# Kernel optimization log

Hardware: AMD Instinct MI355X
Metric: run time of the kernel (lower is better)

## Reference

```python
import jax, jax.numpy as jnp
import numpy as np
import math

B, S, H = 2, 2048, 2048
NQ, NKV, HD = 16, 4, 128
THETA = 10000.0


def rotate_half(x):
    x1, x2 = jnp.split(x, 2, axis=-1)
    return jnp.concatenate([-x2, x1], axis=-1)


def rope_cos_sin(position_ids, dim, base, dtype):
    # inv_freq: (dim/2,)
    inv_freq = 1.0 / (base ** (jnp.arange(0, dim, 2, dtype=jnp.float32) / dim))
    freqs = position_ids.astype(jnp.float32)[..., None] * inv_freq  # (B, S, dim/2)
    emb = jnp.concatenate([freqs, freqs], axis=-1)  # (B, S, dim)
    return jnp.cos(emb).astype(dtype), jnp.sin(emb).astype(dtype)


def setup_inputs() -> dict:
    key = jax.random.key(0)
    ks = jax.random.split(key, 5)
    hidden_states = jax.random.normal(ks[0], (B, S, H), dtype=jnp.float32)
    position_ids = jnp.broadcast_to(jnp.arange(S, dtype=jnp.int32)[None, :], (B, S))
    sc = 0.02
    wq = jax.random.normal(ks[1], (NQ * HD, H), dtype=jnp.float32) * sc
    wk = jax.random.normal(ks[2], (NKV * HD, H), dtype=jnp.float32) * sc
    wv = jax.random.normal(ks[3], (NKV * HD, H), dtype=jnp.float32) * sc
    wo = jax.random.normal(ks[4], (H, NQ * HD), dtype=jnp.float32) * sc
    return {"hidden_states": hidden_states, "position_ids": position_ids,
            "wq": wq, "wk": wk, "wv": wv, "wo": wo}


def reference(hidden_states, position_ids, wq, wk, wv, wo):
    b, s, _ = hidden_states.shape
    n_rep = NQ // NKV
    # QKV projections (no bias)
    q = (hidden_states @ wq.T).reshape(b, s, NQ, HD).transpose(0, 2, 1, 3)   # (b, nq, s, hd)
    k = (hidden_states @ wk.T).reshape(b, s, NKV, HD).transpose(0, 2, 1, 3)  # (b, nkv, s, hd)
    v = (hidden_states @ wv.T).reshape(b, s, NKV, HD).transpose(0, 2, 1, 3)
    # RoPE (full rotary, partial_rotary_factor == 1.0)
    cos, sin = rope_cos_sin(position_ids, HD, THETA, q.dtype)  # (b, s, hd)
    cos = cos[:, None, :, :]
    sin = sin[:, None, :, :]
    q = q * cos + rotate_half(q) * sin
    k = k * cos + rotate_half(k) * sin
    # repeat_kv for GQA: (b, nkv, s, hd) -> (b, nq, s, hd)
    k = jnp.repeat(k, n_rep, axis=1)
    v = jnp.repeat(v, n_rep, axis=1)
    # scores (b, nq, s, s)
    scores = jnp.einsum('bhqd,bhkd->bhqk', q, k) / math.sqrt(HD)
    causal = jnp.triu(jnp.full((s, s), -jnp.inf, dtype=scores.dtype), k=1)
    scores = scores + causal
    probs = jax.nn.softmax(scores.astype(jnp.float32), axis=-1).astype(q.dtype)
    out = jnp.einsum('bhqk,bhkd->bhqd', probs, v)  # (b, nq, s, hd)
    out = out.transpose(0, 2, 1, 3).reshape(b, s, NQ * HD)
    return out @ wo.T
```

## Files before the change

### kernel.cpp

```cpp
#include <hip/hip_runtime.h>
#include <hip/hip_bf16.h>
#include <cstdint>

typedef unsigned short u16;
typedef __attribute__((ext_vector_type(4))) float f32x4;
typedef __attribute__((ext_vector_type(8))) short s16x8;
typedef __attribute__((ext_vector_type(4))) unsigned int u32x4;
typedef __attribute__((ext_vector_type(2))) unsigned int u32x2;
typedef __attribute__((ext_vector_type(4))) unsigned short u16x4;

#define MFMA16(a, b, c) __builtin_amdgcn_mfma_f32_16x16x32_bf16(a, b, c, 0, 0, 0)
#define GLOAD16(g, l) __builtin_amdgcn_global_load_lds((const __attribute__((address_space(1))) void*)(g), (__attribute__((address_space(3))) void*)(l), 16, 0, 0)

__device__ __forceinline__ u16 f2bf(float f) {
    union { float f; uint32_t u; } v{f};
    uint32_t r = v.u + 0x7FFF + ((v.u >> 16) & 1);
    return (u16)(r >> 16);
}

__global__ void cast_f32_bf16(const float* __restrict__ in, u16* __restrict__ out, int n4) {
    int i = blockIdx.x * 256 + threadIdx.x;
    if (i >= n4) return;
    float4 f = ((const float4*)in)[i];
    u16x4 o = { f2bf(f.x), f2bf(f.y), f2bf(f.z), f2bf(f.w) };
    ((u16x4*)out)[i] = o;
}

__global__ void rope_table_k(const int* __restrict__ pos, float* __restrict__ ct, float* __restrict__ st) {
    int i = blockIdx.x * 256 + threadIdx.x;
    int j = i & 63;
    int bs = i >> 6;
    float p = (float)pos[bs];
    float invf = powf(10000.0f, -(float)j * (1.0f / 64.0f));
    float ang = p * invf;
    ct[i] = cosf(ang);
    st[i] = sinf(ang);
}

__global__ __launch_bounds__(256) void gemm_bt(const u16* __restrict__ A, const u16* __restrict__ Bw,
                                               float* __restrict__ C, int M, int N, int K) {
    __shared__ u16 As[128 * 64];
    __shared__ u16 Bs[128 * 64];
    const int tid = threadIdx.x;
    const int lane = tid & 63, wid = tid >> 6;
    const int g = lane >> 4, r = lane & 15;

    const int gx = gridDim.x, nwg = gx * gridDim.y;
    int lid = blockIdx.y * gx + blockIdx.x;
    int swz = (lid % 8) * (nwg / 8) + lid / 8;
    const int bxi = swz % gx, byi = swz / gx;

    const size_t bm = (size_t)byi * 128, bn = (size_t)bxi * 128;
    const int wr = (wid >> 1) * 64, wc = (wid & 1) * 64;

    const int srow = wid * 32 + (lane >> 3);
    const int schunk = (lane & 7) ^ ((lane >> 3) & 7);
    const u16* aSrc = A + (bm + srow) * (size_t)K + schunk * 8;
    const u16* bSrc = Bw + (bn + srow) * (size_t)K + schunk * 8;
    u16* aDst = As + wid * 2048;
    u16* bDst = Bs + wid * 2048;

    f32x4 acc[4][4] = {};
    for (int kt = 0; kt < K; kt += 64) {
#pragma unroll
        for (int j = 0; j < 4; ++j) {
            GLOAD16(aSrc + (size_t)(j * 8) * K + kt, aDst + j * 512);
            GLOAD16(bSrc + (size_t)(j * 8) * K + kt, bDst + j * 512);
        }
        __syncthreads();
        s16x8 af[4][2], bfr[4][2];
#pragma unroll
        for (int m = 0; m < 4; ++m)
#pragma unroll
            for (int kk = 0; kk < 2; ++kk) {
                int rowa = wr + m * 16 + r;
                af[m][kk] = *(const s16x8*)(As + rowa * 64 + (((kk * 4 + g) ^ (rowa & 7)) << 3));
                int rowb = wc + m * 16 + r;
                bfr[m][kk] = *(const s16x8*)(Bs + rowb * 64 + (((kk * 4 + g) ^ (rowb & 7)) << 3));
            }
#pragma unroll
        for (int m = 0; m < 4; ++m)
#pragma unroll
            for (int n = 0; n < 4; ++n) {
                acc[m][n] = MFMA16(af[m][0], bfr[n][0], acc[m][n]);
                acc[m][n] = MFMA16(af[m][1], bfr[n][1], acc[m][n]);
            }
        __syncthreads();
    }
#pragma unroll
    for (int m = 0; m < 4; ++m)
#pragma unroll
        for (int n = 0; n < 4; ++n)
#pragma unroll
            for (int i = 0; i < 4; ++i) {
                size_t row = bm + wr + m * 16 + g * 4 + i;
                size_t col = bn + wc + n * 16 + r;
                C[row * N + col] = acc[m][n][i];
            }
}

__global__ void rope_scatter_k(const float* __restrict__ qkv, const float* __restrict__ ct,
                               const float* __restrict__ st, u16* __restrict__ Qb,
                               u16* __restrict__ Kb, u16* __restrict__ Vb) {
    int bs = blockIdx.y;
    int col = blockIdx.x * 256 + threadIdx.x;
    int b = bs >> 11, s = bs & 2047;
    const float* rowp = qkv + (size_t)bs * 3072;
    float x = rowp[col];
    int d = col & 127;
    if (col >= 2560) {
        int h = (col - 2560) >> 7;
        Vb[(((size_t)(b * 4 + h) * 2048 + s) << 7) + d] = f2bf(x);
    } else {
        int j = d & 63;
        float c = ct[(bs << 6) + j], sn = st[(bs << 6) + j];
        float other = rowp[(col & ~127) + (d ^ 64)];
        float res = (d < 64) ? (x * c - other * sn) : (x * c + other * sn);
        if (col < 2048) {
            int h = col >> 7;
            Qb[(((size_t)(b * 16 + h) * 2048 + s) << 7) + d] = f2bf(res);
        } else {
            int h = (col - 2048) >> 7;
            Kb[(((size_t)(b * 4 + h) * 2048 + s) << 7) + d] = f2bf(res);
        }
    }
}

__global__ __launch_bounds__(256, 2) void attn_k(const u16* __restrict__ Qb, const u16* __restrict__ Kb,
                                                 const u16* __restrict__ Vb, u16* __restrict__ Ob) {
    __shared__ char smem[49152];
    u16* Ksh = (u16*)smem;
    u16* Vts = (u16*)(smem + 16384);
    char* Pall = smem + 32768;
    const int tid = threadIdx.x;
    const int lane = tid & 63, w = tid >> 6;
    const int g = lane >> 4, r = lane & 15;

    const int lid = blockIdx.y * gridDim.x + blockIdx.x;
    const int cpy = lid >> 8, p = lid & 255;
    const int bh = p & 31;
    const int qblk = cpy ? (7 - (p >> 5)) : ((p >> 5) + 8);

    const int b = bh >> 4, h = bh & 15;
    const int hkv = h >> 2;
    const int q0 = qblk * 128;
    const u16* Qh = Qb + ((size_t)(b * 16 + h) << 18);
    const u16* Kh = Kb + ((size_t)(b * 4 + hkv) << 18);
    const u16* Vh = Vb + ((size_t)(b * 4 + hkv) << 18);

    s16x8 qf[2][4];
#pragma unroll
    for (int qq = 0; qq < 2; ++qq)
#pragma unroll
        for (int c = 0; c < 4; ++c)
            qf[qq][c] = *(const s16x8*)(Qh + (size_t)(q0 + qq * 64 + w * 16 + r) * 128 + c * 32 + g * 8);

    f32x4 o[2][8] = {};
    float mrun[2] = {-1e30f, -1e30f};
    float lrun[2] = {0.f, 0.f};
    const int fmax[2] = { q0 + w * 16 + 15, q0 + 64 + w * 16 + 15 };

    const int ntiles = 2 * qblk + 2;
    const int krow0 = tid >> 4, kch = tid & 15;
    const int vdc = tid & 15, vkvp = tid >> 4;

    u32x4 kpr[4], var[2], vbr[2];
#pragma unroll
    for (int it = 0; it < 4; ++it)
        kpr[it] = *(const u32x4*)(Kh + (size_t)(krow0 + it * 16) * 128 + kch * 8);
#pragma unroll
    for (int it = 0; it < 2; ++it) {
        int kv2 = (vkvp + it * 16) * 2;
        var[it] = *(const u32x4*)(Vh + (size_t)kv2 * 128 + vdc * 8);
        vbr[it] = *(const u32x4*)(Vh + (size_t)(kv2 + 1) * 128 + vdc * 8);
    }

    for (int t = 0; t < ntiles; ++t) {
        const int kv0 = t * 64;
        __syncthreads();
#pragma unroll
        for (int it = 0; it < 4; ++it) {
            int row = krow0 + it * 16;
            *(u32x4*)((char*)Ksh + row * 256 + ((kch ^ (row & 7)) << 4)) = kpr[it];
        }
#pragma unroll
        for (int it = 0; it < 2; ++it) {
            int kv2 = (vkvp + it * 16) * 2;
            const u16* p0 = (const u16*)&var[it];
            const u16* p1 = (const u16*)&vbr[it];
#pragma unroll
            for (int j = 0; j < 8; ++j) {
                int d = vdc * 8 + j;
                unsigned int val = (unsigned int)p0[j] | ((unsigned int)p1[j] << 16);
                *(unsigned int*)((char*)Vts +
                    ((d * 128 + kv2 * 2) ^ ((((d & 7) ^ ((d >> 3) & 7))) << 4))) = val;
            }
        }
        __syncthreads();
        if (t + 1 < ntiles) {
            const int kn = kv0 + 64;
#pragma unroll
            for (int it = 0; it < 4; ++it)
                kpr[it] = *(const u32x4*)(Kh + (size_t)(kn + krow0 + it * 16) * 128 + kch * 8);
#pragma unroll
            for (int it = 0; it < 2; ++it) {
                int kv2 = kn + (vkvp + it * 16) * 2;
                var[it] = *(const u32x4*)(Vh + (size_t)kv2 * 128 + vdc * 8);
                vbr[it] = *(const u32x4*)(Vh + (size_t)(kv2 + 1) * 128 + vdc * 8);
            }
        }
        f32x4 st4[2][4];
#pragma unroll
        for (int ts = 0; ts < 4; ++ts) {
            int row = ts * 16 + r;
            s16x8 kf[4];
#pragma unroll
            for (int c = 0; c < 4; ++c)
                kf[c] = *(const s16x8*)((const char*)Ksh + row * 256 + (((c * 4 + g) ^ (row & 7)) << 4));
            f32x4 a0 = {}, a1 = {};
            if (kv0 <= fmax[0])
#pragma unroll
                for (int c = 0; c < 4; ++c) a0 = MFMA16(kf[c], qf[0][c], a0);
            if (kv0 <= fmax[1])
#pragma unroll
                for (int c = 0; c < 4; ++c) a1 = MFMA16(kf[c], qf[1][c], a1);
            st4[0][ts] = a0;
            st4[1][ts] = a1;
        }
#pragma unroll
        for (int qq = 0; qq < 2; ++qq) {
            if (kv0 > fmax[qq]) continue;
            const int qg = q0 + qq * 64 + w * 16 + r;
            float sv[16];
            float mtile = -1e30f;
#pragma unroll
            for (int ts = 0; ts < 4; ++ts)
#pragma unroll
                for (int i = 0; i < 4; ++i) {
                    int kvg = kv0 + ts * 16 + g * 4 + i;
                    float s = st4[qq][ts][i] * 0.08838834764831845f;
                    s = (kvg > qg) ? -1e30f : s;
                    sv[ts * 4 + i] = s;
                    mtile = fmaxf(mtile, s);
                }
            mtile = fmaxf(mtile, __shfl_xor(mtile, 16));
            mtile = fmaxf(mtile, __shfl_xor(mtile, 32));
            float mnew = fmaxf(mrun[qq], mtile);
            float corr = __expf(mrun[qq] - mnew);
            float psum = 0.f;
            unsigned int pw[8];
#pragma unroll
            for (int ts = 0; ts < 4; ++ts) {
                float p0 = __expf(sv[ts * 4 + 0] - mnew);
                float p1 = __expf(sv[ts * 4 + 1] - mnew);
                float p2 = __expf(sv[ts * 4 + 2] - mnew);
                float p3 = __expf(sv[ts * 4 + 3] - mnew);
                psum += (p0 + p1) + (p2 + p3);
                pw[ts * 2 + 0] = (unsigned int)f2bf(p0) | ((unsigned int)f2bf(p1) << 16);
                pw[ts * 2 + 1] = (unsigned int)f2bf(p2) | ((unsigned int)f2bf(p3) << 16);
            }
            psum += __shfl_xor(psum, 16);
            psum += __shfl_xor(psum, 32);
            lrun[qq] = lrun[qq] * corr + psum;
            mrun[qq] = mnew;
#pragma unroll
            for (int dsb = 0; dsb < 8; ++dsb)
#pragma unroll
                for (int i = 0; i < 4; ++i) o[qq][dsb][i] *= corr;
            char* pbase = Pall + (w * 2 + qq) * 2048;
#pragma unroll
            for (int ts = 0; ts < 4; ++ts) {
                int chunk = (ts * 2 + (g >> 1)) ^ (r & 7);
                u32x2 val = { pw[ts * 2], pw[ts * 2 + 1] };
                *(u32x2*)(pbase + r * 128 + chunk * 16 + (g & 1) * 8) = val;
            }
        }
        asm volatile("s_waitcnt lgkmcnt(0)" ::: "memory");
#pragma unroll
        for (int c = 0; c < 2; ++c) {
            s16x8 vf[8];
#pragma unroll
            for (int dsb = 0; dsb < 8; ++dsb) {
                int d = dsb * 16 + r;
                vf[dsb] = *(const s16x8*)((const char*)Vts + d * 128 +
                    ((((c * 4 + g) ^ (d & 7) ^ ((d >> 3) & 7))) << 4));
            }
#pragma unroll
            for (int qq = 0; qq < 2; ++qq) {
                if (kv0 > fmax[qq]) continue;
                s16x8 pf = *(const s16x8*)(Pall + (w * 2 + qq) * 2048 + r * 128 +
                                           (((c * 4 + g) ^ (r & 7)) << 4));
#pragma unroll
                for (int dsb = 0; dsb < 8; ++dsb)
                    o[qq][dsb] = MFMA16(vf[dsb], pf, o[qq][dsb]);
            }
        }
    }
    __syncthreads();
#pragma unroll
    for (int qq = 0; qq < 2; ++qq) {
        float linv = 1.0f / lrun[qq];
        char* obase = smem + (w << 13) + (qq << 12);
#pragma unroll
        for (int dsb = 0; dsb < 8; ++dsb)
#pragma unroll
            for (int i = 0; i < 4; ++i) {
                int d = dsb * 16 + g * 4 + i;
                *(u16*)(obase + r * 256 + d * 2) = f2bf(o[qq][dsb][i] * linv);
            }
    }
    asm volatile("s_waitcnt lgkmcnt(0)" ::: "memory");
    const int rr = lane >> 2, cbo = (lane & 3) * 32;
#pragma unroll
    for (int qq = 0; qq < 2; ++qq) {
        char* obase = smem + (w << 13) + (qq << 12);
        size_t oidx = ((size_t)b * 2048 + q0 + qq * 64 + w * 16 + rr) * 2048 + h * 128 + cbo;
#pragma unroll
        for (int p2 = 0; p2 < 4; ++p2) {
            u32x4 vv = *(const u32x4*)(obase + rr * 256 + cbo * 2 + p2 * 16);
            *(u32x4*)(Ob + oidx + p2 * 8) = vv;
        }
    }
}

extern "C" void kernel_launch(void* const* d_in, const int* in_sizes, int n_in,
                              void* d_out, int out_size, void* d_ws, size_t ws_size,
                              hipStream_t stream) {
    const float* hidden = (const float*)d_in[0];
    const int* pos = (const int*)d_in[1];
    const float* wq = (const float*)d_in[2];
    const float* wk = (const float*)d_in[3];
    const float* wv = (const float*)d_in[4];
    const float* wo = (const float*)d_in[5];
    float* out = (float*)d_out;

    char* ws = (char*)d_ws;
    size_t off = 0;
    auto alloc = [&](size_t bytes) { char* p = ws + off; off += (bytes + 255) & ~255ULL; return p; };
    u16* Xb   = (u16*)alloc(8388608ULL * 2);
    u16* WB   = (u16*)alloc(6291456ULL * 2);
    u16* WoB  = (u16*)alloc(4194304ULL * 2);
    float* QKV = (float*)alloc(12582912ULL * 4);
    u16* Qb   = (u16*)alloc(8388608ULL * 2);
    u16* Kb   = (u16*)alloc(2097152ULL * 2);
    u16* Vb   = (u16*)alloc(2097152ULL * 2);
    u16* Ab   = (u16*)alloc(8388608ULL * 2);
    float* ctab = (float*)alloc(262144ULL * 4);
    float* stab = (float*)alloc(262144ULL * 4);

    cast_f32_bf16<<<8192, 256, 0, stream>>>(hidden, Xb, 2097152);
    cast_f32_bf16<<<4096, 256, 0, stream>>>(wq, WB, 1048576);
    cast_f32_bf16<<<1024, 256, 0, stream>>>(wk, WB + 4194304, 262144);
    cast_f32_bf16<<<1024, 256, 0, stream>>>(wv, WB + 5242880, 262144);
    cast_f32_bf16<<<4096, 256, 0, stream>>>(wo, WoB, 1048576);
    rope_table_k<<<1024, 256, 0, stream>>>(pos, ctab, stab);
    gemm_bt<<<dim3(24, 32), 256, 0, stream>>>(Xb, WB, QKV, 4096, 3072, 2048);
    rope_scatter_k<<<dim3(12, 4096), 256, 0, stream>>>(QKV, ctab, stab, Qb, Kb, Vb);
    attn_k<<<dim3(16, 32), 256, 0, stream>>>(Qb, Kb, Vb, Ab);
    gemm_bt<<<dim3(16, 32), 256, 0, stream>>>(Ab, WoB, out, 4096, 2048, 2048);
}
```

Measured before the change: 263.8 us.

## Fuse RoPE and QKV head scatter into the QKV GEMM epilogue

The QKV projection GEMM now stages its output tile as bf16 in a swizzled shared-memory buffer. Half of the threads then apply RoPE per token row and write directly into the Q/K/V head-major bf16 buffers. This removes the fp32 QKV intermediate, its round trip through global memory, and the separate scatter kernel launch. In exchange, the epilogue is serialized over 128 threads with per-thread row stores. RoPE is also applied to bf16-rounded values rather than fp32 ones.

```diff
diff --git a/kernel.cpp b/kernel.cpp
--- a/kernel.cpp
+++ b/kernel.cpp
@@ -16,6 +16,11 @@
     union { float f; uint32_t u; } v{f};
     uint32_t r = v.u + 0x7FFF + ((v.u >> 16) & 1);
     return (u16)(r >> 16);
+}
+__device__ __forceinline__ float bf2f(u16 b) {
+    union { uint32_t u; float f; } v;
+    v.u = ((uint32_t)b) << 16;
+    return v.f;
 }
 
 __global__ void cast_f32_bf16(const float* __restrict__ in, u16* __restrict__ out, int n4) {
@@ -37,10 +42,15 @@
     st[i] = sinf(ang);
 }
 
+template <int FUSE>
 __global__ __launch_bounds__(256) void gemm_bt(const u16* __restrict__ A, const u16* __restrict__ Bw,
-                                               float* __restrict__ C, int M, int N, int K) {
-    __shared__ u16 As[128 * 64];
-    __shared__ u16 Bs[128 * 64];
+                                               float* __restrict__ C, int M, int N, int K,
+                                               const float* __restrict__ ct, const float* __restrict__ st,
+                                               u16* __restrict__ Qb, u16* __restrict__ Kb,
+                                               u16* __restrict__ Vb) {
+    __shared__ u16 Sh[128 * 128];
+    u16* As = Sh;
+    u16* Bs = Sh + 8192;
     const int tid = threadIdx.x;
     const int lane = tid & 63, wid = tid >> 6;
     const int g = lane >> 4, r = lane & 15;
@@ -87,41 +97,72 @@
             }
         __syncthreads();
     }
+    if (FUSE == 0) {
+#pragma unroll
+        for (int m = 0; m < 4; ++m)
+#pragma unroll
+            for (int n = 0; n < 4; ++n)
+#pragma unroll
+                for (int i = 0; i < 4; ++i) {
+                    size_t row = bm + wr + m * 16 + g * 4 + i;
+                    size_t col = bn + wc + n * 16 + r;
+                    C[row * N + col] = acc[m][n][i];
+                }
+        return;
+    }
 #pragma unroll
     for (int m = 0; m < 4; ++m)
 #pragma unroll
         for (int n = 0; n < 4; ++n)
 #pragma unroll
             for (int i = 0; i < 4; ++i) {
-                size_t row = bm + wr + m * 16 + g * 4 + i;
-                size_t col = bn + wc + n * 16 + r;
-                C[row * N + col] = acc[m][n][i];
-            }
-}
-
-__global__ void rope_scatter_k(const float* __restrict__ qkv, const float* __restrict__ ct,
-                               const float* __restrict__ st, u16* __restrict__ Qb,
-                               u16* __restrict__ Kb, u16* __restrict__ Vb) {
-    int bs = blockIdx.y;
-    int col = blockIdx.x * 256 + threadIdx.x;
-    int b = bs >> 11, s = bs & 2047;
-    const float* rowp = qkv + (size_t)bs * 3072;
-    float x = rowp[col];
-    int d = col & 127;
-    if (col >= 2560) {
-        int h = (col - 2560) >> 7;
-        Vb[(((size_t)(b * 4 + h) * 2048 + s) << 7) + d] = f2bf(x);
-    } else {
-        int j = d & 63;
-        float c = ct[(bs << 6) + j], sn = st[(bs << 6) + j];
-        float other = rowp[(col & ~127) + (d ^ 64)];
-        float res = (d < 64) ? (x * c - other * sn) : (x * c + other * sn);
-        if (col < 2048) {
-            int h = col >> 7;
-            Qb[(((size_t)(b * 16 + h) * 2048 + s) << 7) + d] = f2bf(res);
+                int rowl = wr + m * 16 + g * 4 + i;
+                int col = wc + n * 16 + r;
+                int c4 = col >> 3;
+                *(u16*)((char*)Sh + rowl * 256 + (((c4 ^ (rowl & 15))) << 4) + ((col & 7) << 1)) =
+                    f2bf(acc[m][n][i]);
+            }
+    __syncthreads();
+    if (tid < 128) {
+        const int rowl = tid;
+        const size_t tok = bm + rowl;
+        const int b = (int)(tok >> 11), s = (int)(tok & 2047);
+        const int hb = bxi;
+        u16* dst;
+        if (hb < 16)      dst = Qb + (((size_t)(b * 16 + hb) * 2048 + s) << 7);
+        else if (hb < 20) dst = Kb + (((size_t)(b * 4 + (hb - 16)) * 2048 + s) << 7);
+        else              dst = Vb + (((size_t)(b * 4 + (hb - 20)) * 2048 + s) << 7);
+        const char* tb = (const char*)Sh + rowl * 256;
+        if (hb < 20) {
+            const float* ctr = ct + tok * 64;
+            const float* str = st + tok * 64;
+#pragma unroll
+            for (int c4 = 0; c4 < 8; ++c4) {
+                u32x4 lo4 = *(const u32x4*)(tb + ((c4 ^ (rowl & 15)) << 4));
+                u32x4 hi4 = *(const u32x4*)(tb + (((c4 + 8) ^ (rowl & 15)) << 4));
+                const u16* lo = (const u16*)&lo4;
+                const u16* hi = (const u16*)&hi4;
+                u16x4 o0, o1, o2, o3;
+                u16* olo[2] = { (u16*)&o0, (u16*)&o1 };
+                u16* ohi[2] = { (u16*)&o2, (u16*)&o3 };
+#pragma unroll
+                for (int j = 0; j < 8; ++j) {
+                    float c = ctr[c4 * 8 + j], sn = str[c4 * 8 + j];
+                    float xl = bf2f(lo[j]), xh = bf2f(hi[j]);
+                    olo[j >> 2][j & 3] = f2bf(xl * c - xh * sn);
+                    ohi[j >> 2][j & 3] = f2bf(xh * c + xl * sn);
+                }
+                *(u16x4*)(dst + c4 * 8) = o0;
+                *(u16x4*)(dst + c4 * 8 + 4) = o1;
+                *(u16x4*)(dst + 64 + c4 * 8) = o2;
+                *(u16x4*)(dst + 64 + c4 * 8 + 4) = o3;
+            }
         } else {
-            int h = (col - 2048) >> 7;
-            Kb[(((size_t)(b * 4 + h) * 2048 + s) << 7) + d] = f2bf(res);
+#pragma unroll
+            for (int c4 = 0; c4 < 16; ++c4) {
+                u32x4 v4 = *(const u32x4*)(tb + ((c4 ^ (rowl & 15)) << 4));
+                *(u32x4*)(dst + c4 * 8) = v4;
+            }
         }
     }
 }
@@ -340,7 +381,6 @@
     u16* Xb   = (u16*)alloc(8388608ULL * 2);
     u16* WB   = (u16*)alloc(6291456ULL * 2);
     u16* WoB  = (u16*)alloc(4194304ULL * 2);
-    float* QKV = (float*)alloc(12582912ULL * 4);
     u16* Qb   = (u16*)alloc(8388608ULL * 2);
     u16* Kb   = (u16*)alloc(2097152ULL * 2);
     u16* Vb   = (u16*)alloc(2097152ULL * 2);
@@ -354,8 +394,9 @@
     cast_f32_bf16<<<1024, 256, 0, stream>>>(wv, WB + 5242880, 262144);
     cast_f32_bf16<<<4096, 256, 0, stream>>>(wo, WoB, 1048576);
     rope_table_k<<<1024, 256, 0, stream>>>(pos, ctab, stab);
-    gemm_bt<<<dim3(24, 32), 256, 0, stream>>>(Xb, WB, QKV, 4096, 3072, 2048);
-    rope_scatter_k<<<dim3(12, 4096), 256, 0, stream>>>(QKV, ctab, stab, Qb, Kb, Vb);
+    gemm_bt<1><<<dim3(24, 32), 256, 0, stream>>>(Xb, WB, nullptr, 4096, 3072, 2048,
+                                                 ctab, stab, Qb, Kb, Vb);
     attn_k<<<dim3(16, 32), 256, 0, stream>>>(Qb, Kb, Vb, Ab);
-    gemm_bt<<<dim3(16, 32), 256, 0, stream>>>(Ab, WoB, out, 4096, 2048, 2048);
-}
+    gemm_bt<0><<<dim3(16, 32), 256, 0, stream>>>(Ab, WoB, out, 4096, 2048, 2048,
+                                                 nullptr, nullptr, nullptr, nullptr, nullptr);
+}
```

New measurement: 249.6 us. 5.4% less time.
